# Kernel tuning notes

Measured on AMD Instinct MI355X. Metric: run time of the kernel, lower is better.

## Reference

```python
import jax, jax.numpy as jnp
import numpy as np

COMMITMENT_WEIGHT = 0.25


def _vq_layer(residual, codebook):
    """One euclidean VQ layer: nearest-codeword lookup + straight-through.
    residual: [B,T,D], codebook: [K,D].
    Returns (q_st [B,T,D], idx [B,T], commit_loss scalar).
    """
    B, T, D = residual.shape
    flat = residual.reshape(-1, D)  # [N,D]
    d2 = (jnp.sum(flat * flat, axis=-1, keepdims=True)
          - 2.0 * flat @ codebook.T
          + jnp.sum(codebook * codebook, axis=-1))  # [N,K]
    idx = jnp.argmin(d2, axis=-1)                   # [N]
    q = codebook[idx].reshape(B, T, D)
    # straight-through estimator (as in vector_quantize_pytorch)
    q_st = residual + jax.lax.stop_gradient(q - residual)
    commit_loss = COMMITMENT_WEIGHT * jnp.mean(
        (jax.lax.stop_gradient(q) - residual) ** 2)
    return q_st, idx.reshape(B, T), commit_loss


def setup_inputs() -> dict:
    key = jax.random.key(0)
    ks = jax.random.split(key, 9)
    D = 768
    sizes = [2, 4, 8, 16, 32, 64, 128, 256]
    inp = {"x": jax.random.normal(ks[0], (32, 2048, D), dtype=jnp.float32)}
    for i, K in enumerate(sizes):
        inp[f"cb{i}"] = jax.random.normal(ks[i + 1], (K, D), dtype=jnp.float32)
    return inp


def reference(x, cb0, cb1, cb2, cb3, cb4, cb5, cb6, cb7):
    codebooks = [cb0, cb1, cb2, cb3, cb4, cb5, cb6, cb7]
    residual = x
    quantized = jnp.zeros_like(x)
    all_indices = []
    total_commit_loss = jnp.float32(0.0)
    for cb in codebooks:  # fixed 8 structurally-distinct layers
        q, idx, commit = _vq_layer(residual, cb)
        quantized = quantized + q
        residual = residual - q
        all_indices.append(idx)
        total_commit_loss = total_commit_loss + commit
    all_indices = jnp.stack(all_indices, axis=-1)  # [B,T,num_layers]
    return quantized, all_indices, total_commit_loss
```

## Files before the change

kernel.cpp:

```cpp
#include <hip/hip_runtime.h>
#include <stdint.h>

#define NTOK 65536
#define DIM  768
#define NCB  512
#define NC   510
#define TAU  0.75f

typedef _Float16 f16x8 __attribute__((ext_vector_type(8)));
typedef float f32x4 __attribute__((ext_vector_type(4)));

#define WS_C32   0u
#define WS_CHI   1572864u
#define WS_CNORM 3145728u
#define WS_G     3147776u
#define WS_IDX   4196352u
#define WS_PART  6293504u
#define WS_S     8388608u
#define S_BYTES  67108864u

__device__ __forceinline__ void gl_lds16(const void* g, void* l){
  __builtin_amdgcn_global_load_lds(
      (const __attribute__((address_space(1))) unsigned int*)g,
      (__attribute__((address_space(3))) unsigned int*)l,
      16, 0, 0);
}

__global__ void k_prep(const float* __restrict__ cb0, const float* __restrict__ cb1,
                       const float* __restrict__ cb2, const float* __restrict__ cb3,
                       const float* __restrict__ cb4, const float* __restrict__ cb5,
                       const float* __restrict__ cb6, const float* __restrict__ cb7,
                       char* __restrict__ ws){
  const int r = blockIdx.x, t = threadIdx.x;
  const float* srcs[8] = {cb0,cb1,cb2,cb3,cb4,cb5,cb6,cb7};
  const int off[8] = {0,2,6,14,30,62,126,254};
  const int KK[8]  = {2,4,8,16,32,64,128,256};
  const float* src = nullptr;
#pragma unroll
  for (int l=0;l<8;l++)
    if (r >= off[l] && r < off[l]+KK[l]) src = srcs[l] + (size_t)(r - off[l]) * DIM;
  float* C32 = (float*)(ws + WS_C32);
  _Float16* Chi = (_Float16*)(ws + WS_CHI);
  double ss = 0.0;
#pragma unroll
  for (int i=0;i<3;i++){
    const int e = t + i*256;
    const float v = src ? src[e] : 0.f;
    C32[(size_t)r*DIM + e] = v;
    Chi[(size_t)r*DIM + e] = (_Float16)v;
    ss += (double)v * (double)v;
  }
  __shared__ double red[256];
  red[t] = ss; __syncthreads();
  for (int sdown=128; sdown>0; sdown>>=1){
    if (t < sdown) red[t] += red[t+sdown];
    __syncthreads();
  }
  if (t == 0){
    float* cnp = (float*)(ws + WS_CNORM);
    cnp[r] = (r < NC) ? (float)red[0] : 1e30f;
  }
}

__global__ void k_gram(char* __restrict__ ws){
  const int i = blockIdx.x, t = threadIdx.x;
  const float* __restrict__ C32 = (const float*)(ws + WS_C32);
  __shared__ float row[DIM];
  for (int e=t; e<DIM; e+=256) row[e] = C32[(size_t)i*DIM + e];
  __syncthreads();
  float* __restrict__ G = (float*)(ws + WS_G);
  for (int j=t; j<NCB; j+=256){
    const float4* cj = (const float4*)(C32 + (size_t)j*DIM);
    double d = 0.0;
    for (int k=0; k<DIM/4; k++){
      const float4 b = cj[k];
      d += (double)row[4*k]*(double)b.x + (double)row[4*k+1]*(double)b.y
         + (double)row[4*k+2]*(double)b.z + (double)row[4*k+3]*(double)b.w;
    }
    G[(size_t)i*NCB + j] = (float)d;
  }
}

__global__ __launch_bounds__(256, 3) void k_gemm(const float* __restrict__ x,
                                                 const char* __restrict__ ws,
                                                 _Float16* __restrict__ S){
  __shared__ __align__(16) char smem[49152];
  const int t = threadIdx.x, lane = t & 63, w = t >> 6;
  const int wm = w >> 1, wn = w & 1;
  const int bid = blockIdx.x;
  const int xcd = bid & 7, jj = bid >> 3;
  const int mt = xcd*64 + (jj >> 2), nt = jj & 3;
  const _Float16* __restrict__ Chi = (const _Float16*)(ws + WS_CHI);

  f32x4 acc[4][4];
#pragma unroll
  for (int i=0;i<4;i++)
#pragma unroll
    for (int j=0;j<4;j++) acc[i][j] = {0.f,0.f,0.f,0.f};

  for (int kt=0; kt<12; kt++){
#pragma unroll
    for (int i8=0;i8<8;i8++){
      const int r0 = w*32 + i8*4;
      const int row = r0 + (lane>>4);
      const int g = lane & 15;
      const int sg = g ^ (((row&7)<<1) | ((row>>3)&1));
      const size_t go = (size_t)(mt*128 + row)*DIM + (size_t)kt*64 + sg*4;
      gl_lds16(x + go, smem + r0*256);
    }
#pragma unroll
    for (int c4=0;c4<4;c4++){
      const int r0 = w*32 + c4*8;
      const int rloc = r0 + (lane>>3);
      const int jsrc = (lane&7) ^ (rloc&7);
      const size_t go = (size_t)(nt*128 + rloc)*DIM + (size_t)kt*64 + jsrc*8;
      gl_lds16(Chi + go, smem + 32768 + r0*128);
    }
    __syncthreads();
#pragma unroll
    for (int kk=0; kk<2; kk++){
      f16x8 fa[4], fb[4];
#pragma unroll
      for (int mf=0;mf<4;mf++){
        const int m = wm*64 + mf*16 + (lane&15);
        const int maskm = ((m&7)<<1) | ((m>>3)&1);
        const int ch = kk*4 + (lane>>4);
        const int g0 = (2*ch) ^ maskm;
        const f32x4 lo = *(const f32x4*)(smem + m*256 + g0*16);
        const f32x4 hi = *(const f32x4*)(smem + m*256 + (g0^1)*16);
        f16x8 r;
        r[0]=(_Float16)lo[0]; r[1]=(_Float16)lo[1]; r[2]=(_Float16)lo[2]; r[3]=(_Float16)lo[3];
        r[4]=(_Float16)hi[0]; r[5]=(_Float16)hi[1]; r[6]=(_Float16)hi[2]; r[7]=(_Float16)hi[3];
        fa[mf] = r;
      }
#pragma unroll
      for (int nf=0;nf<4;nf++){
        const int c = wn*64 + nf*16 + (lane&15);
        const uint bb = (uint)(32768 + c*128 + ((((kk<<2)+(lane>>4)) ^ (c&7))*16));
        fb[nf] = *(const f16x8*)(smem + bb);
      }
#pragma unroll
      for (int mf=0;mf<4;mf++)
#pragma unroll
        for (int nf=0;nf<4;nf++)
          acc[mf][nf] = __builtin_amdgcn_mfma_f32_16x16x32_f16(fa[mf], fb[nf], acc[mf][nf], 0,0,0);
    }
    __syncthreads();
  }

#pragma unroll
  for (int mf=0;mf<4;mf++)
#pragma unroll
    for (int nf=0;nf<4;nf++){
      const f32x4 v = acc[mf][nf];
      const int col  = nt*128 + wn*64 + nf*16 + (lane&15);
      const int row0 = mt*128 + wm*64 + mf*16 + ((lane>>4)<<2);
#pragma unroll
      for (int e=0;e<4;e++)
        S[(size_t)(row0+e)*NCB + col] = (_Float16)v[e];
    }
}

template<int FUSED>
__global__ __launch_bounds__(256, 4) void k_chain(const float* __restrict__ x,
                                                  const _Float16* __restrict__ S,
                                                  char* __restrict__ ws,
                                                  float* __restrict__ out,
                                                  float* __restrict__ part){
  const int t = threadIdx.x, lane = t & 63, w = t >> 6;
  const size_t tok = (size_t)blockIdx.x*4 + w;
  const float* __restrict__ cn  = (const float*)(ws + WS_CNORM);
  const float* __restrict__ G   = (const float*)(ws + WS_G);
  const float* __restrict__ C32 = (const float*)(ws + WS_C32);

  float xv[12], rv[12];
  {
    const float4* xp = (const float4*)(x + tok*DIM + lane*12);
#pragma unroll
    for (int q=0;q<3;q++){
      const float4 v = xp[q];
      xv[q*4]=v.x; xv[q*4+1]=v.y; xv[q*4+2]=v.z; xv[q*4+3]=v.w;
    }
  }
#pragma unroll
  for (int i=0;i<12;i++) rv[i] = xv[i];

  float sv[8], s0[8];
  {
    const uint* sp = (const uint*)(S + tok*NCB);
#pragma unroll
    for (int j=0;j<4;j++){
      union { uint u; _Float16 h[2]; } cv;
      cv.u = sp[j*64 + lane];
      sv[2*j]   = (float)cv.h[0];
      sv[2*j+1] = (float)cv.h[1];
    }
  }
#pragma unroll
  for (int k=0;k<8;k++) s0[k] = sv[k];

  float ssq = 0.f;

  for (int l=0; l<8; ++l){
    const int cs = (2<<l) - 2;
    const int ce = cs + (2<<l);
    float bv = 3e38f; int bc = 0x7fffffff;
#pragma unroll
    for (int j=0;j<4;j++){
      const float2 c2 = *(const float2*)(cn + j*128 + lane*2);
      const int c0 = j*128 + lane*2;
      const float sA = (c0   >= cs && c0   < ce) ? (c2.x - 2.f*sv[2*j])   : 3e38f;
      const float sB = (c0+1 >= cs && c0+1 < ce) ? (c2.y - 2.f*sv[2*j+1]) : 3e38f;
      if (sA < bv){ bv = sA; bc = c0; }
      if (sB < bv){ bv = sB; bc = c0+1; }
    }
#pragma unroll
    for (int d=1; d<64; d<<=1){
      const float ov = __shfl_xor(bv, d);
      const int   oc = __shfl_xor(bc, d);
      if (ov < bv || (ov == bv && oc < bc)){ bv = ov; bc = oc; }
    }
    int bm = 0;
#pragma unroll
    for (int j=0;j<4;j++){
      const float2 c2 = *(const float2*)(cn + j*128 + lane*2);
      const int c0 = j*128 + lane*2;
      const float sA = (c0   >= cs && c0   < ce) ? (c2.x - 2.f*sv[2*j])   : 3e38f;
      const float sB = (c0+1 >= cs && c0+1 < ce) ? (c2.y - 2.f*sv[2*j+1]) : 3e38f;
      if (sA <= bv + TAU) bm |= 1 << (2*j);
      if (sB <= bv + TAU) bm |= 1 << (2*j+1);
    }
    const unsigned long long lmask = __ballot(bm != 0);
    const int b0 = __ffsll((long long)lmask) - 1;
    const int bm0 = __shfl(bm, b0);
    const bool multi = (__popcll(lmask) > 1) || ((bm0 & (bm0-1)) != 0);

    int mc = bc;
    if (multi){
      double bve = 1e300; int bce = 0x7fffffff;
      unsigned long long Lm = lmask;
      while (Lm){
        const int b = __ffsll((long long)Lm) - 1; Lm &= Lm - 1;
        int mbits = __shfl(bm, b);
        while (mbits){
          const int k = __ffs(mbits) - 1; mbits &= mbits - 1;
          const int c = (k>>1)*128 + b*2 + (k&1);
          const float dkv = __shfl(s0[k] - sv[k], b);
          const float* __restrict__ crow = C32 + (size_t)c*DIM + lane*12;
          double dd = 0.0;
#pragma unroll
          for (int q=0;q<3;q++){
            const float4 v = *(const float4*)(crow + q*4);
            dd += (double)xv[q*4]*v.x + (double)xv[q*4+1]*v.y
                + (double)xv[q*4+2]*v.z + (double)xv[q*4+3]*v.w;
          }
#pragma unroll
          for (int d=1; d<64; d<<=1) dd += __shfl_xor(dd, d);
          const double se = (double)cn[c] - 2.0*(dd - (double)dkv);
          if (se < bve || (se == bve && c < bce)){ bve = se; bce = c; }
        }
      }
      mc = bce;
    }

    if (lane == 0){
      if (FUSED) out[(size_t)NTOK*DIM + tok*8 + l] = (float)(mc - cs);
      else       ((int*)(ws + WS_IDX))[tok*8 + l]  = mc - cs;
    }
    if (l < 7){
      const float* __restrict__ gr = G + (size_t)mc*NCB;
#pragma unroll
      for (int j=0;j<4;j++){
        const float2 g2 = *(const float2*)(gr + j*128 + lane*2);
        sv[2*j] -= g2.x; sv[2*j+1] -= g2.y;
      }
    }
    if (FUSED){
      const float* __restrict__ cw = C32 + (size_t)mc*DIM + lane*12;
#pragma unroll
      for (int q=0;q<3;q++){
        const float4 v = *(const float4*)(cw + q*4);
        rv[q*4]-=v.x; rv[q*4+1]-=v.y; rv[q*4+2]-=v.z; rv[q*4+3]-=v.w;
      }
#pragma unroll
      for (int i=0;i<12;i++) ssq += rv[i]*rv[i];
    }
  }

  if (FUSED){
    float* op = out + tok*DIM + lane*12;
#pragma unroll
    for (int q=0;q<3;q++){
      float4 v;
      v.x = xv[q*4]-rv[q*4]; v.y = xv[q*4+1]-rv[q*4+1];
      v.z = xv[q*4+2]-rv[q*4+2]; v.w = xv[q*4+3]-rv[q*4+3];
      *(float4*)(op + q*4) = v;
    }
#pragma unroll
    for (int d=32; d>0; d>>=1) ssq += __shfl_down(ssq, d);
    __shared__ float bs[4];
    if (lane == 0) bs[w] = ssq;
    __syncthreads();
    if (t == 0) part[blockIdx.x] = bs[0]+bs[1]+bs[2]+bs[3];
  }
}

__global__ __launch_bounds__(512) void k_fin(const float* __restrict__ x,
                                             char* __restrict__ ws,
                                             float* __restrict__ out,
                                             float* __restrict__ part){
  const int t = threadIdx.x, lane = t & 63, w = t >> 6;
  const size_t tok = (size_t)blockIdx.x * 8 + w;
  const int off[8] = {0,2,6,14,30,62,126,254};
  const int* __restrict__ idxw = (const int*)(ws + WS_IDX);
  const float* __restrict__ C32 = (const float*)(ws + WS_C32);
  int loc[8];
#pragma unroll
  for (int l=0;l<8;l++) loc[l] = idxw[tok*8 + l];
  if (lane < 8) out[(size_t)NTOK*DIM + tok*8 + lane] = (float)idxw[tok*8 + lane];

  const float4* __restrict__ xr = (const float4*)(x + tok*DIM);
  float4* __restrict__ qr = (float4*)(out + tok*DIM);
  const float4* crow[8];
#pragma unroll
  for (int l=0;l<8;l++) crow[l] = (const float4*)(C32 + (size_t)(loc[l] + off[l])*DIM);
  float ssq = 0.f;
#pragma unroll
  for (int i=0;i<3;i++){
    const int e4 = i*64 + lane;
    const float4 xv = xr[e4];
    float rx = xv.x, ry = xv.y, rz = xv.z, rw = xv.w;
    float qx = 0.f, qy = 0.f, qz = 0.f, qw = 0.f;
#pragma unroll
    for (int l=0;l<8;l++){
      const float4 cv = crow[l][e4];
      rx -= cv.x; ry -= cv.y; rz -= cv.z; rw -= cv.w;
      qx += cv.x; qy += cv.y; qz += cv.z; qw += cv.w;
      ssq += rx*rx + ry*ry + rz*rz + rw*rw;
    }
    float4 q; q.x = qx; q.y = qy; q.z = qz; q.w = qw;
    qr[e4] = q;
  }
#pragma unroll
  for (int d=32; d>0; d>>=1) ssq += __shfl_down(ssq, d);
  __shared__ float bsum[8];
  if (lane == 0) bsum[w] = ssq;
  __syncthreads();
  if (t == 0){
    float s2 = 0.f;
#pragma unroll
    for (int j=0;j<8;j++) s2 += bsum[j];
    part[blockIdx.x] = s2;
  }
}

__global__ void k_loss(const float* __restrict__ part, int n,
                       float* __restrict__ out){
  const int t = threadIdx.x;
  double s = 0.0;
  for (int i=t; i<n; i+=256) s += (double)part[i];
  __shared__ double red[256];
  red[t] = s; __syncthreads();
  for (int d=128; d>0; d>>=1){
    if (t < d) red[t] += red[t+d];
    __syncthreads();
  }
  if (t == 0)
    out[(size_t)NTOK*DIM + (size_t)NTOK*8] =
      (float)(0.25 * red[0] / (double)((size_t)NTOK * DIM));
}

extern "C" void kernel_launch(void* const* d_in, const int* in_sizes, int n_in,
                              void* d_out, int out_size, void* d_ws, size_t ws_size,
                              hipStream_t stream){
  const float* x = (const float*)d_in[0];
  char* ws = (char*)d_ws;
  float* out = (float*)d_out;
  float* part = (float*)(ws + WS_PART);
  const bool fused = ws_size >= (size_t)WS_S + (size_t)S_BYTES;
  _Float16* Sp = fused ? (_Float16*)(ws + WS_S) : (_Float16*)out;

  k_prep<<<512, 256, 0, stream>>>((const float*)d_in[1], (const float*)d_in[2],
                                  (const float*)d_in[3], (const float*)d_in[4],
                                  (const float*)d_in[5], (const float*)d_in[6],
                                  (const float*)d_in[7], (const float*)d_in[8], ws);
  k_gram<<<512, 256, 0, stream>>>(ws);
  k_gemm<<<2048, 256, 0, stream>>>(x, ws, Sp);
  if (fused){
    k_chain<1><<<16384, 256, 0, stream>>>(x, Sp, ws, out, part);
    k_loss<<<1, 256, 0, stream>>>(part, 16384, out);
  } else {
    k_chain<0><<<16384, 256, 0, stream>>>(x, Sp, ws, out, part);
    k_fin<<<8192, 512, 0, stream>>>(x, ws, out, part);
    k_loss<<<1, 256, 0, stream>>>(part, 8192, out);
  }
}
```

Before: 442.9 us.

## Derive commit loss from distances and drop per-token x reload in chain

The GEMM kernel now also computes per-token squared norms of x from the shared-memory tiles. The chain kernel uses those norms to build the commitment loss algebraically: it accumulates the running residual norm from the selected minimum distances instead of tracking the residual vector. x is loaded only on the rare exact-refinement path, and the output is the sum of the selected codewords. This removes the full x read from the chain kernel and caches codebook norms in registers. The cost is extra work in the GEMM, and a loss now built from fp16-derived dot products, which may drift numerically.

```diff
diff --git a/kernel.cpp b/kernel.cpp
--- a/kernel.cpp
+++ b/kernel.cpp
@@ -16,6 +16,9 @@
 #define WS_G     3147776u
 #define WS_IDX   4196352u
 #define WS_PART  6293504u
+#define WS_XN    6match_placeholder
+#undef WS_XN
+#define WS_XN    6359040u
 #define WS_S     8388608u
 #define S_BYTES  67108864u
 
@@ -83,7 +86,8 @@
 
 __global__ __launch_bounds__(256, 3) void k_gemm(const float* __restrict__ x,
                                                  const char* __restrict__ ws,
-                                                 _Float16* __restrict__ S){
+                                                 _Float16* __restrict__ S,
+                                                 float* __restrict__ xn){
   __shared__ __align__(16) char smem[49152];
   const int t = threadIdx.x, lane = t & 63, w = t >> 6;
   const int wm = w >> 1, wn = w & 1;
@@ -98,6 +102,8 @@
 #pragma unroll
     for (int j=0;j<4;j++) acc[i][j] = {0.f,0.f,0.f,0.f};
 
+  float xs = 0.f;
+
   for (int kt=0; kt<12; kt++){
 #pragma unroll
     for (int i8=0;i8<8;i8++){
@@ -117,6 +123,14 @@
       gl_lds16(Chi + go, smem + 32768 + r0*128);
     }
     __syncthreads();
+    if (nt == 0){
+      const int rr = t & 127, hf = t >> 7;
+#pragma unroll
+      for (int g=0; g<8; g++){
+        const f32x4 v = *(const f32x4*)(smem + rr*256 + hf*128 + g*16);
+        xs += v[0]*v[0] + v[1]*v[1] + v[2]*v[2] + v[3]*v[3];
+      }
+    }
 #pragma unroll
     for (int kk=0; kk<2; kk++){
       f16x8 fa[4], fb[4];
@@ -148,6 +162,12 @@
     __syncthreads();
   }
 
+  if (nt == 0){
+    ((float*)smem)[t] = xs;
+    __syncthreads();
+    if (t < 128) xn[mt*128 + t] = ((float*)smem)[t] + ((float*)smem)[t + 128];
+  }
+
 #pragma unroll
   for (int mf=0;mf<4;mf++)
 #pragma unroll
@@ -166,26 +186,15 @@
                                                   const _Float16* __restrict__ S,
                                                   char* __restrict__ ws,
                                                   float* __restrict__ out,
-                                                  float* __restrict__ part){
+                                                  float* __restrict__ part,
+                                                  const float* __restrict__ xn){
   const int t = threadIdx.x, lane = t & 63, w = t >> 6;
   const size_t tok = (size_t)blockIdx.x*4 + w;
   const float* __restrict__ cn  = (const float*)(ws + WS_CNORM);
   const float* __restrict__ G   = (const float*)(ws + WS_G);
   const float* __restrict__ C32 = (const float*)(ws + WS_C32);
 
-  float xv[12], rv[12];
-  {
-    const float4* xp = (const float4*)(x + tok*DIM + lane*12);
-#pragma unroll
-    for (int q=0;q<3;q++){
-      const float4 v = xp[q];
-      xv[q*4]=v.x; xv[q*4+1]=v.y; xv[q*4+2]=v.z; xv[q*4+3]=v.w;
-    }
-  }
-#pragma unroll
-  for (int i=0;i<12;i++) rv[i] = xv[i];
-
-  float sv[8], s0[8];
+  float sv[8], s0[8], cnv[8];
   {
     const uint* sp = (const uint*)(S + tok*NCB);
 #pragma unroll
@@ -194,23 +203,27 @@
       cv.u = sp[j*64 + lane];
       sv[2*j]   = (float)cv.h[0];
       sv[2*j+1] = (float)cv.h[1];
+      const float2 c2 = *(const float2*)(cn + j*128 + lane*2);
+      cnv[2*j] = c2.x; cnv[2*j+1] = c2.y;
     }
   }
 #pragma unroll
   for (int k=0;k<8;k++) s0[k] = sv[k];
 
-  float ssq = 0.f;
-
+  int mcs[8];
+  float h = FUSED ? xn[tok] : 0.f;
+  float tot = 0.f;
+
+#pragma unroll
   for (int l=0; l<8; ++l){
     const int cs = (2<<l) - 2;
     const int ce = cs + (2<<l);
     float bv = 3e38f; int bc = 0x7fffffff;
 #pragma unroll
     for (int j=0;j<4;j++){
-      const float2 c2 = *(const float2*)(cn + j*128 + lane*2);
       const int c0 = j*128 + lane*2;
-      const float sA = (c0   >= cs && c0   < ce) ? (c2.x - 2.f*sv[2*j])   : 3e38f;
-      const float sB = (c0+1 >= cs && c0+1 < ce) ? (c2.y - 2.f*sv[2*j+1]) : 3e38f;
+      const float sA = (c0   >= cs && c0   < ce) ? (cnv[2*j]   - 2.f*sv[2*j])   : 3e38f;
+      const float sB = (c0+1 >= cs && c0+1 < ce) ? (cnv[2*j+1] - 2.f*sv[2*j+1]) : 3e38f;
       if (sA < bv){ bv = sA; bc = c0; }
       if (sB < bv){ bv = sB; bc = c0+1; }
     }
@@ -223,10 +236,9 @@
     int bm = 0;
 #pragma unroll
     for (int j=0;j<4;j++){
-      const float2 c2 = *(const float2*)(cn + j*128 + lane*2);
       const int c0 = j*128 + lane*2;
-      const float sA = (c0   >= cs && c0   < ce) ? (c2.x - 2.f*sv[2*j])   : 3e38f;
-      const float sB = (c0+1 >= cs && c0+1 < ce) ? (c2.y - 2.f*sv[2*j+1]) : 3e38f;
+      const float sA = (c0   >= cs && c0   < ce) ? (cnv[2*j]   - 2.f*sv[2*j])   : 3e38f;
+      const float sB = (c0+1 >= cs && c0+1 < ce) ? (cnv[2*j+1] - 2.f*sv[2*j+1]) : 3e38f;
       if (sA <= bv + TAU) bm |= 1 << (2*j);
       if (sB <= bv + TAU) bm |= 1 << (2*j+1);
     }
@@ -236,37 +248,47 @@
     const bool multi = (__popcll(lmask) > 1) || ((bm0 & (bm0-1)) != 0);
 
     int mc = bc;
+    float ssel = bv;
     if (multi){
+      float xv[12];
+      {
+        const float4* xp = (const float4*)(x + tok*DIM + lane*12);
+#pragma unroll
+        for (int q=0;q<3;q++){
+          const float4 v = xp[q];
+          xv[q*4]=v.x; xv[q*4+1]=v.y; xv[q*4+2]=v.z; xv[q*4+3]=v.w;
+        }
+      }
       double bve = 1e300; int bce = 0x7fffffff;
       unsigned long long Lm = lmask;
       while (Lm){
         const int b = __ffsll((long long)Lm) - 1; Lm &= Lm - 1;
-        int mbits = __shfl(bm, b);
-        while (mbits){
-          const int k = __ffs(mbits) - 1; mbits &= mbits - 1;
-          const int c = (k>>1)*128 + b*2 + (k&1);
-          const float dkv = __shfl(s0[k] - sv[k], b);
-          const float* __restrict__ crow = C32 + (size_t)c*DIM + lane*12;
-          double dd = 0.0;
-#pragma unroll
-          for (int q=0;q<3;q++){
-            const float4 v = *(const float4*)(crow + q*4);
-            dd += (double)xv[q*4]*v.x + (double)xv[q*4+1]*v.y
-                + (double)xv[q*4+2]*v.z + (double)xv[q*4+3]*v.w;
+        const int mbits = __shfl(bm, b);
+#pragma unroll
+        for (int k=0;k<8;k++){
+          if (mbits & (1<<k)){
+            const int c = (k>>1)*128 + b*2 + (k&1);
+            const float dkv = __shfl(s0[k] - sv[k], b);
+            const float* __restrict__ crow = C32 + (size_t)c*DIM + lane*12;
+            double dd = 0.0;
+#pragma unroll
+            for (int q=0;q<3;q++){
+              const float4 v = *(const float4*)(crow + q*4);
+              dd += (double)xv[q*4]*v.x + (double)xv[q*4+1]*v.y
+                  + (double)xv[q*4+2]*v.z + (double)xv[q*4+3]*v.w;
+            }
+#pragma unroll
+            for (int d=1; d<64; d<<=1) dd += __shfl_xor(dd, d);
+            const double se = (double)cn[c] - 2.0*(dd - (double)dkv);
+            if (se < bve || (se == bve && c < bce)){ bve = se; bce = c; }
           }
-#pragma unroll
-          for (int d=1; d<64; d<<=1) dd += __shfl_xor(dd, d);
-          const double se = (double)cn[c] - 2.0*(dd - (double)dkv);
-          if (se < bve || (se == bve && c < bce)){ bve = se; bce = c; }
         }
       }
       mc = bce;
-    }
-
-    if (lane == 0){
-      if (FUSED) out[(size_t)NTOK*DIM + tok*8 + l] = (float)(mc - cs);
-      else       ((int*)(ws + WS_IDX))[tok*8 + l]  = mc - cs;
-    }
+      ssel = (float)bve;
+    }
+    mcs[l] = mc;
+    if (FUSED){ h += ssel; tot += h; }
     if (l < 7){
       const float* __restrict__ gr = G + (size_t)mc*NCB;
 #pragma unroll
@@ -275,33 +297,45 @@
         sv[2*j] -= g2.x; sv[2*j+1] -= g2.y;
       }
     }
-    if (FUSED){
-      const float* __restrict__ cw = C32 + (size_t)mc*DIM + lane*12;
-#pragma unroll
-      for (int q=0;q<3;q++){
-        const float4 v = *(const float4*)(cw + q*4);
-        rv[q*4]-=v.x; rv[q*4+1]-=v.y; rv[q*4+2]-=v.z; rv[q*4+3]-=v.w;
-      }
-#pragma unroll
-      for (int i=0;i<12;i++) ssq += rv[i]*rv[i];
-    }
   }
 
   if (FUSED){
+    float q[12];
+#pragma unroll
+    for (int i=0;i<12;i++) q[i] = 0.f;
+#pragma unroll
+    for (int l=0;l<8;l++){
+      const float* __restrict__ cw = C32 + (size_t)mcs[l]*DIM + lane*12;
+#pragma unroll
+      for (int qq=0;qq<3;qq++){
+        const float4 v = *(const float4*)(cw + qq*4);
+        q[qq*4]+=v.x; q[qq*4+1]+=v.y; q[qq*4+2]+=v.z; q[qq*4+3]+=v.w;
+      }
+    }
     float* op = out + tok*DIM + lane*12;
 #pragma unroll
-    for (int q=0;q<3;q++){
-      float4 v;
-      v.x = xv[q*4]-rv[q*4]; v.y = xv[q*4+1]-rv[q*4+1];
-      v.z = xv[q*4+2]-rv[q*4+2]; v.w = xv[q*4+3]-rv[q*4+3];
-      *(float4*)(op + q*4) = v;
-    }
-#pragma unroll
-    for (int d=32; d>0; d>>=1) ssq += __shfl_down(ssq, d);
+    for (int qq=0;qq<3;qq++){
+      float4 v; v.x=q[qq*4]; v.y=q[qq*4+1]; v.z=q[qq*4+2]; v.w=q[qq*4+3];
+      *(float4*)(op + qq*4) = v;
+    }
+    if (lane == 0){
+      float4 i0, i1;
+      i0.x=(float)(mcs[0]-0);   i0.y=(float)(mcs[1]-2);   i0.z=(float)(mcs[2]-6);   i0.w=(float)(mcs[3]-14);
+      i1.x=(float)(mcs[4]-30);  i1.y=(float)(mcs[5]-62);  i1.z=(float)(mcs[6]-126); i1.w=(float)(mcs[7]-254);
+      *(float4*)(out + (size_t)NTOK*DIM + tok*8)     = i0;
+      *(float4*)(out + (size_t)NTOK*DIM + tok*8 + 4) = i1;
+    }
     __shared__ float bs[4];
-    if (lane == 0) bs[w] = ssq;
+    if (lane == 0) bs[w] = tot;
     __syncthreads();
     if (t == 0) part[blockIdx.x] = bs[0]+bs[1]+bs[2]+bs[3];
+  } else {
+    if (lane == 0){
+      int* idxw = (int*)(ws + WS_IDX);
+      const int offs[8] = {0,2,6,14,30,62,126,254};
+#pragma unroll
+      for (int l=0;l<8;l++) idxw[tok*8 + l] = mcs[l] - offs[l];
+    }
   }
 }
 
@@ -377,6 +411,7 @@
   char* ws = (char*)d_ws;
   float* out = (float*)d_out;
   float* part = (float*)(ws + WS_PART);
+  float* xn   = (float*)(ws + WS_XN);
   const bool fused = ws_size >= (size_t)WS_S + (size_t)S_BYTES;
   _Float16* Sp = fused ? (_Float16*)(ws + WS_S) : (_Float16*)out;
 
@@ -385,12 +420,12 @@
                                   (const float*)d_in[5], (const float*)d_in[6],
                                   (const float*)d_in[7], (const float*)d_in[8], ws);
   k_gram<<<512, 256, 0, stream>>>(ws);
-  k_gemm<<<2048, 256, 0, stream>>>(x, ws, Sp);
+  k_gemm<<<2048, 256, 0, stream>>>(x, ws, Sp, xn);
   if (fused){
-    k_chain<1><<<16384, 256, 0, stream>>>(x, Sp, ws, out, part);
+    k_chain<1><<<16384, 256, 0, stream>>>(x, Sp, ws, out, part, xn);
     k_loss<<<1, 256, 0, stream>>>(part, 16384, out);
   } else {
-    k_chain<0><<<16384, 256, 0, stream>>>(x, Sp, ws, out, part);
+    k_chain<0><<<16384, 256, 0, stream>>>(x, Sp, ws, out, part, xn);
     k_fin<<<8192, 512, 0, stream>>>(x, ws, out, part);
     k_loss<<<1, 256, 0, stream>>>(part, 8192, out);
   }
```

Result: no change. 448.6 us (+1.3%).
